# Kernel optimization log

Measured on AMD Instinct MI355X. Metric: run time of the kernel, lower is better.

Reference implementation:

```python
import jax, jax.numpy as jnp
import numpy as np

THETA = 0.7
KS = 3          # deformable-conv kernel size
N = KS * KS     # 9 sampling points


def setup_inputs() -> dict:
    key = jax.random.key(0)
    k = jax.random.split(key, 7)
    B, C, H, W = 2, 256, 64, 64
    x = jax.random.normal(k[0], (B, C, H, W), jnp.float32)
    # offset-predicting conv (3x3, pad 1), 2*N output channels; small init so offsets are sane
    p_w = jax.random.normal(k[1], (2 * N, C, 3, 3), jnp.float32) * 0.01
    p_b = jax.random.normal(k[2], (2 * N,), jnp.float32) * 0.01
    # modulation conv (3x3, pad 1), N output channels
    m_w = jax.random.normal(k[3], (N, C, 3, 3), jnp.float32) * 0.01
    m_b = jnp.zeros((N,), jnp.float32)
    # final deform conv weight (applied as ks x ks, stride ks over the unfolded map), no bias
    dconv_w = jax.random.normal(k[4], (256, C, KS, KS), jnp.float32) * 0.05
    # central-difference conv raw weight, shape (Cout, Cin, 1, 5), no bias
    cdc_w = jax.random.normal(k[5], (256, C, 1, 5), jnp.float32) * 0.05
    return {"x": x, "p_w": p_w, "p_b": p_b, "m_w": m_w, "m_b": m_b,
            "dconv_w": dconv_w, "cdc_w": cdc_w}


def _conv2d(x, w, pad):
    return jax.lax.conv_general_dilated(
        x, w, window_strides=(1, 1), padding=pad,
        dimension_numbers=("NCHW", "OIHW", "NCHW"))


def deform_conv(x, p_w, p_b, m_w, m_b, dconv_w):
    B, C, H, W = x.shape
    same = [(1, 1), (1, 1)]
    offset = _conv2d(x, p_w, same) + p_b[None, :, None, None]          # [B,2N,H,W]
    m = jax.nn.sigmoid(_conv2d(x, m_w, same) + m_b[None, :, None, None])  # [B,N,H,W]

    xp = jnp.pad(x, ((0, 0), (0, 0), (1, 1), (1, 1)))  # zero padding 1
    Hp, Wp = H + 2, W + 2

    # p = p_0 + p_n + offset  (x = row coord, y = col coord; torch meshgrid 'ij')
    p_n_x = jnp.repeat(jnp.arange(-1, 2, dtype=x.dtype), 3)   # [-1,-1,-1,0,0,0,1,1,1]
    p_n_y = jnp.tile(jnp.arange(-1, 2, dtype=x.dtype), 3)     # [-1,0,1,-1,0,1,-1,0,1]
    rows = jnp.arange(1, H + 1, dtype=x.dtype)                # p_0_x
    cols = jnp.arange(1, W + 1, dtype=x.dtype)                # p_0_y
    px = offset[:, :N] + p_n_x[None, :, None, None] + rows[None, None, :, None]
    py = offset[:, N:] + p_n_y[None, :, None, None] + cols[None, None, None, :]
    px = jnp.transpose(px, (0, 2, 3, 1))  # [B,H,W,N]
    py = jnp.transpose(py, (0, 2, 3, 1))

    # integer corners from UNCLAMPED p (detached), as in the original
    fx = jnp.floor(jax.lax.stop_gradient(px))
    fy = jnp.floor(jax.lax.stop_gradient(py))
    qx0 = jnp.clip(fx, 0, Hp - 1)
    qy0 = jnp.clip(fy, 0, Wp - 1)
    qx1 = jnp.clip(fx + 1, 0, Hp - 1)
    qy1 = jnp.clip(fy + 1, 0, Wp - 1)

    # clamp p before computing bilinear weights (original order)
    pxc = jnp.clip(px, 0, Hp - 1)
    pyc = jnp.clip(py, 0, Wp - 1)
    g_lt = (1 + (qx0 - pxc)) * (1 + (qy0 - pyc))
    g_rb = (1 - (qx1 - pxc)) * (1 - (qy1 - pyc))
    g_lb = (1 + (qx0 - pxc)) * (1 - (qy1 - pyc))
    g_rt = (1 - (qx1 - pxc)) * (1 + (qy0 - pyc))

    xf = xp.reshape(B, C, Hp * Wp)

    def gather(qx, qy):
        idx = (qx.astype(jnp.int32) * Wp + qy.astype(jnp.int32)).reshape(B, 1, -1)
        return jnp.take_along_axis(xf, idx, axis=2).reshape(B, C, H, W, N)

    x_off = (g_lt[:, None] * gather(qx0, qy0)
             + g_rb[:, None] * gather(qx1, qy1)
             + g_lb[:, None] * gather(qx0, qy1)
             + g_rt[:, None] * gather(qx1, qy0))          # [B,C,H,W,N]
    x_off = x_off * jnp.transpose(m, (0, 2, 3, 1))[:, None]  # modulation broadcast over C

    # conv(ksxks, stride ks) over the unfolded map == contraction over the N taps;
    # tap n = 3r + c corresponds to kernel position (r, c)
    w = dconv_w.reshape(dconv_w.shape[0], C, N)
    return jnp.einsum("bchwn,ocn->bohw", x_off, w)


def cdc_conv(x, cdc_w):
    Co, Ci = cdc_w.shape[0], cdc_w.shape[1]
    z = jnp.zeros((Co, Ci, 1), cdc_w.dtype)
    wk = jnp.concatenate(
        [z, cdc_w[:, :, :, 0], z, cdc_w[:, :, :, 1], cdc_w[:, :, :, 2],
         cdc_w[:, :, :, 3], z, cdc_w[:, :, :, 4], z], axis=2
    ).reshape(Co, Ci, 3, 3)
    out_normal = _conv2d(x, wk, [(1, 1), (1, 1)])
    kdiff = cdc_w.sum(axis=(2, 3))[:, :, None, None]
    out_diff = _conv2d(x, kdiff, [(0, 0), (0, 0)])
    return out_normal - THETA * out_diff


def reference(x, p_w, p_b, m_w, m_b, dconv_w, cdc_w):
    out_dc = jax.nn.relu(deform_conv(x, p_w, p_b, m_w, m_b, dconv_w))
    out_cdc = jax.nn.relu(cdc_conv(x, cdc_w))
    return jnp.concatenate([out_dc, out_cdc], axis=1)  # [B,512,H,W]
```

## Files before the change

kernel.cpp:

```cpp
#include <hip/hip_runtime.h>
#include <hip/hip_bf16.h>
#include <math.h>

#define XT_BSTRIDE (66*66*256)
#define THETA_ 0.7f

typedef unsigned short u16;
typedef __attribute__((ext_vector_type(8))) short bf16x8;
typedef __attribute__((ext_vector_type(4))) float f32x4;

#define GLOAD16(gp, lp) __builtin_amdgcn_global_load_lds( \
    (const __attribute__((address_space(1))) unsigned int*)(gp), \
    (__attribute__((address_space(3))) unsigned int*)(lp), 16, 0, 0)

__device__ __forceinline__ float bf2f(u16 v) {
  union { unsigned u; float f; } x; x.u = ((unsigned)v) << 16; return x.f;
}
__device__ __forceinline__ u16 f2bf(float f) {
  __hip_bfloat16 h = __float2bfloat16(f);
  return *(u16*)&h;
}

__device__ __forceinline__ size_t swz_idx(int row, int k, int KT) {
  int kt = k >> 6, kc = (k >> 3) & 7, kj = k & 7;
  return (size_t)row * KT + kt * 64 + ((kc ^ (row & 7)) << 3) + kj;
}

__global__ __launch_bounds__(256) void prep(
    const float* __restrict__ x, const float* __restrict__ p_w,
    const float* __restrict__ m_w, const float* __restrict__ dconv_w,
    const float* __restrict__ cdc_w, u16* __restrict__ xTb,
    u16* __restrict__ W1t, u16* __restrict__ Wdt, u16* __restrict__ Wct) {
  int blk = blockIdx.x;
  if (blk < 512) {
    int cg = blk & 3;
    int h  = (blk >> 2) & 63;
    int b  = blk >> 8;
    __shared__ float tile[64][65];
    const float* xp = x + ((size_t)(b * 256 + cg * 64)) * 4096 + h * 64;
#pragma unroll
    for (int j = 0; j < 16; j++) {
      int idx = j * 256 + threadIdx.x;
      int ci = idx >> 6, w = idx & 63;
      tile[ci][w] = xp[(size_t)ci * 4096 + w];
    }
    __syncthreads();
    u16* xo = xTb + (size_t)b * XT_BSTRIDE + ((h + 1) * 66 + 1) * 256 + cg * 64;
#pragma unroll
    for (int j = 0; j < 16; j++) {
      int idx = j * 256 + threadIdx.x;
      int w = idx >> 6, ci = idx & 63;
      xo[(size_t)w * 256 + ci] = f2bf(tile[ci][w]);
    }
    return;
  }
  if (blk < 1032) {
    int i = (blk - 512) * 256 + threadIdx.x;
    if (i >= 133120) return;
    int c = i & 255;
    int j = i >> 8;
    int b = (j >= 260) ? 1 : 0;
    int r = j - b * 260;
    int hp, wp;
    if (r < 66)       { hp = 0;        wp = r; }
    else if (r < 132) { hp = 65;       wp = r - 66; }
    else if (r < 196) { hp = r - 131;  wp = 0; }
    else              { hp = r - 195;  wp = 65; }
    xTb[(size_t)b * XT_BSTRIDE + (hp * 66 + wp) * 256 + c] = 0;
    return;
  }
  int i = (blk - 1032) * 256 + threadIdx.x;
  if (i < 73728) {
    int o = i / 2304, k = i % 2304;
    int kp = k >> 8, c = k & 255;
    float v = 0.f;
    if (o < 18)      v = p_w[((size_t)o * 256 + c) * 9 + kp];
    else if (o < 27) v = m_w[((size_t)(o - 18) * 256 + c) * 9 + kp];
    W1t[swz_idx(o, k, 2304)] = f2bf(v);
    return;
  }
  int j = i - 73728;
  if (j < 589824) {
    int o = j / 2304, k = j % 2304;
    int n = k >> 8, c = k & 255;
    Wdt[swz_idx(o, k, 2304)] = f2bf(dconv_w[((size_t)o * 256 + c) * 9 + n]);
    return;
  }
  int j2 = j - 589824;
  if (j2 < 327680) {
    int o = j2 / 1280, k = j2 % 1280;
    int t = k >> 8, c = k & 255;
    const float* cw = cdc_w + ((size_t)o * 256 + c) * 5;
    float v = cw[t];
    if (t == 2) v -= THETA_ * (cw[0] + cw[1] + cw[2] + cw[3] + cw[4]);
    Wct[swz_idx(o, k, 1280)] = f2bf(v);
  }
}

__global__ __launch_bounds__(256) void sample_params(
    const float* __restrict__ omp, const float* __restrict__ p_b,
    const float* __restrict__ m_b, int4* __restrict__ sidx,
    float4* __restrict__ sg) {
  int i = blockIdx.x * 256 + threadIdx.x;
  if (i >= 73728) return;
  int n = i % 9;
  int p = i / 9;
  int b = p >> 12;
  int hw = p & 4095;
  int h = hw >> 6, w = hw & 63;
  float offx = p_b[n], offy = p_b[9 + n], mraw = m_b[n];
#pragma unroll
  for (int ks = 0; ks < 4; ks++) {
    const float* base = omp + ks * 221184 + b * 110592;
    offx += base[(size_t)n * 4096 + hw];
    offy += base[(size_t)(9 + n) * 4096 + hw];
    mraw += base[(size_t)(18 + n) * 4096 + hw];
  }
  float px = offx + (float)(h + n / 3);
  float py = offy + (float)(w + n % 3);
  float fx = floorf(px), fy = floorf(py);
  float qx0 = fminf(fmaxf(fx, 0.f), 65.f);
  float qy0 = fminf(fmaxf(fy, 0.f), 65.f);
  float qx1 = fminf(fmaxf(fx + 1.f, 0.f), 65.f);
  float qy1 = fminf(fmaxf(fy + 1.f, 0.f), 65.f);
  float pxc = fminf(fmaxf(px, 0.f), 65.f);
  float pyc = fminf(fmaxf(py, 0.f), 65.f);
  float gx0 = 1.f + (qx0 - pxc);
  float gx1 = 1.f - (qx1 - pxc);
  float gy0 = 1.f + (qy0 - pyc);
  float gy1 = 1.f - (qy1 - pyc);
  float m = 1.f / (1.f + expf(-mraw));
  sidx[i] = make_int4((int)qx0 * 66 + (int)qy0, (int)qx1 * 66 + (int)qy1,
                      (int)qx0 * 66 + (int)qy1, (int)qx1 * 66 + (int)qy0);
  sg[i] = make_float4(gx0 * gy0 * m, gx1 * gy1 * m, gx0 * gy1 * m, gx1 * gy0 * m);
}

__global__ __launch_bounds__(256) void gather_Ad(const u16* __restrict__ xTb,
                                                 const int4* __restrict__ sidx,
                                                 const float4* __restrict__ sg,
                                                 u16* __restrict__ Ad) {
  int gid = blockIdx.x * 256 + threadIdx.x;
  int q = gid & 31;
  int s = gid >> 5;
  int p = s / 9, n = s - p * 9;
  int b = p >> 12;
  int4 qi = sidx[s];
  float4 g = sg[s];
  const u16* xb = xTb + (size_t)b * XT_BSTRIDE + q * 8;
  bf16x8 a0 = *(const bf16x8*)(xb + (size_t)qi.x * 256);
  bf16x8 a1 = *(const bf16x8*)(xb + (size_t)qi.y * 256);
  bf16x8 a2 = *(const bf16x8*)(xb + (size_t)qi.z * 256);
  bf16x8 a3 = *(const bf16x8*)(xb + (size_t)qi.w * 256);
  bf16x8 ov;
#pragma unroll
  for (int j = 0; j < 8; j++) {
    float v = g.x * bf2f((u16)a0[j]) + g.y * bf2f((u16)a1[j]) +
              g.z * bf2f((u16)a2[j]) + g.w * bf2f((u16)a3[j]);
    ov[j] = (short)f2bf(v);
  }
  int k = n * 256 + q * 8;
  int kt = k >> 6, kc = (k >> 3) & 7;
  *(bf16x8*)(Ad + (size_t)p * 2304 + kt * 64 + (((kc ^ (p & 7)) << 3))) = ov;
}

template <int KTOT, int MODE>
__device__ __forceinline__ void gemm_body(
    const u16* __restrict__ Asrc, const u16* __restrict__ Bt,
    float* __restrict__ outp, int mt, int nt, int kt0, int nkt,
    u16* As, u16* Bs) {
  const int BN = (MODE == 2) ? 32 : 64;
  const int WM = (MODE == 2) ? 32 : 64;
  const int MF = WM / 16;
  const int OCH0 = (MODE == 1) ? 256 : 0;

  int tid = threadIdx.x;
  int wid = tid >> 6, lane = tid & 63;
  int wr = (MODE == 2) ? wid : (wid >> 1);
  int wc = (MODE == 2) ? 0 : (wid & 1);
  int pbase = mt * 128;
  int obase = nt * BN;
  int l8 = lane >> 3, l7 = lane & 7;
  int lr = lane & 15, lg = lane >> 4;

  f32x4 acc[2][4];
#pragma unroll
  for (int i = 0; i < 2; i++)
#pragma unroll
    for (int j = 0; j < 4; j++) acc[i][j] = {0.f, 0.f, 0.f, 0.f};

  const int dh1[5] = {0, 1, 1, 1, 2}, dw1[5] = {1, 0, 1, 2, 1};

  auto stage = [&](int kt, u16* Ad_, u16* Bd_) {
    if (MODE == 0) {
#pragma unroll
      for (int i = 0; i < 4; i++) {
        int r0 = wid * 32 + i * 8;
        const u16* g = Asrc + (size_t)(pbase + r0 + l8) * KTOT + kt * 64 + (l7 << 3);
        GLOAD16(g, &Ad_[r0 * 64]);
      }
    } else {
      int t = kt >> 2, c0 = (kt & 3) << 6;
      int dh, dw;
      if (MODE == 1) { dh = dh1[t]; dw = dw1[t]; }
      else           { dh = t / 3;  dw = t % 3;  }
#pragma unroll
      for (int i = 0; i < 4; i++) {
        int r0 = wid * 32 + i * 8;
        int r = r0 + l8;
        int p = pbase + r;
        int b = p >> 12, hw = p & 4095, h = hw >> 6, w = hw & 63;
        int chunk = l7 ^ (r & 7);
        const u16* g = Asrc + (size_t)b * XT_BSTRIDE +
                       ((h + dh) * 66 + (w + dw)) * 256 + c0 + (chunk << 3);
        GLOAD16(g, &Ad_[r0 * 64]);
      }
    }
#pragma unroll
    for (int i = 0; i < BN / 32; i++) {
      int o0 = wid * (BN / 4) + i * 8;
      const u16* g = Bt + (size_t)(obase + o0 + l8) * KTOT + kt * 64 + (l7 << 3);
      GLOAD16(g, &Bd_[o0 * 64]);
    }
  };

  stage(kt0, As, Bs);
  __syncthreads();

  for (int it = 0; it < nkt; it++) {
    int cur = it & 1;
    u16* Ac = As + cur * (128 * 64);
    u16* Bc = Bs + cur * (BN * 64);
    if (it + 1 < nkt)
      stage(kt0 + it + 1, As + (cur ^ 1) * (128 * 64), Bs + (cur ^ 1) * (BN * 64));

    bf16x8 av[4][2], bv[2][2];
#pragma unroll
    for (int mf = 0; mf < MF; mf++) {
      int r = wr * WM + mf * 16 + lr;
#pragma unroll
      for (int ks = 0; ks < 2; ks++) {
        int kc = ks * 4 + lg;
        av[mf][ks] = *(const bf16x8*)&Ac[r * 64 + ((kc ^ (r & 7)) << 3)];
      }
    }
#pragma unroll
    for (int nf = 0; nf < 2; nf++) {
      int o = wc * 32 + nf * 16 + lr;
#pragma unroll
      for (int ks = 0; ks < 2; ks++) {
        int kc = ks * 4 + lg;
        bv[nf][ks] = *(const bf16x8*)&Bc[o * 64 + ((kc ^ (o & 7)) << 3)];
      }
    }
#pragma unroll
    for (int nf = 0; nf < 2; nf++)
#pragma unroll
      for (int mf = 0; mf < MF; mf++)
#pragma unroll
        for (int ks = 0; ks < 2; ks++)
          acc[nf][mf] = __builtin_amdgcn_mfma_f32_16x16x32_bf16(
              bv[nf][ks], av[mf][ks], acc[nf][mf], 0, 0, 0);
    __syncthreads();
  }

  if (MODE != 2) {
#pragma unroll
    for (int nf = 0; nf < 2; nf++)
#pragma unroll
      for (int mf = 0; mf < MF; mf++) {
        int p = pbase + wr * WM + mf * 16 + lr;
        int hw = p & 4095, b = p >> 12;
        int og = OCH0 + obase + wc * 32 + nf * 16 + lg * 4;
        f32x4 v = acc[nf][mf];
#pragma unroll
        for (int e = 0; e < 4; e++)
          outp[(size_t)(b * 512 + og + e) * 4096 + hw] = fmaxf(v[e], 0.f);
      }
  } else {
#pragma unroll
    for (int nf = 0; nf < 2; nf++)
#pragma unroll
      for (int mf = 0; mf < 2; mf++) {
        int p = pbase + wr * 32 + mf * 16 + lr;
        int hw = p & 4095, b = p >> 12;
        int o0 = nf * 16 + lg * 4;
        f32x4 v = acc[nf][mf];
#pragma unroll
        for (int e = 0; e < 4; e++) {
          int o = o0 + e;
          if (o < 27)
            outp[(size_t)(b * 27 + o) * 4096 + hw] = v[e];
        }
      }
  }
}

__global__ __launch_bounds__(256) void gemm_offmod(const u16* __restrict__ xTb,
                                                   const u16* __restrict__ W1t,
                                                   float* __restrict__ omp) {
  __shared__ u16 As[2 * 128 * 64];
  __shared__ u16 Bs[2 * 32 * 64];
  int bid = blockIdx.x;
  int xcd = bid & 7;
  int i = bid >> 3;
  int mt = xcd * 8 + (i & 7);
  int ks = i >> 3;
  gemm_body<2304, 2>(xTb, W1t, omp + ks * 221184, mt, 0, ks * 9, 9, As, Bs);
}

__global__ __launch_bounds__(256) void gemm_main(const u16* __restrict__ Ad,
                                                 const u16* __restrict__ xTb,
                                                 const u16* __restrict__ Wdt,
                                                 const u16* __restrict__ Wct,
                                                 float* __restrict__ out) {
  __shared__ u16 As[2 * 128 * 64];
  __shared__ u16 Bs[2 * 64 * 64];
  int bid = blockIdx.x;
  int xcd = bid & 7;
  int i = bid >> 3;
  if (i < 32) {
    int mt = xcd * 8 + (i >> 2);
    int nt = i & 3;
    gemm_body<2304, 0>(Ad, Wdt, out, mt, nt, 0, 36, As, Bs);
  } else {
    i -= 32;
    int mt = xcd * 8 + (i >> 2);
    int nt = i & 3;
    gemm_body<1280, 1>(xTb, Wct, out, mt, nt, 0, 20, As, Bs);
  }
}

extern "C" void kernel_launch(void* const* d_in, const int* in_sizes, int n_in,
                              void* d_out, int out_size, void* d_ws, size_t ws_size,
                              hipStream_t stream) {
  (void)in_sizes; (void)n_in; (void)out_size; (void)ws_size;
  const float* x       = (const float*)d_in[0];
  const float* p_w     = (const float*)d_in[1];
  const float* p_b     = (const float*)d_in[2];
  const float* m_w     = (const float*)d_in[3];
  const float* m_b     = (const float*)d_in[4];
  const float* dconv_w = (const float*)d_in[5];
  const float* cdc_w   = (const float*)d_in[6];
  float* out = (float*)d_out;
  char* ws = (char*)d_ws;

  u16*   xTb  = (u16*)(ws);
  float* omp  = (float*)(ws + 4460544);
  u16*   W1t  = (u16*)(ws + 7999488);
  u16*   Wdt  = (u16*)(ws + 8146944);
  u16*   Wct  = (u16*)(ws + 9326592);
  int4*  sidx = (int4*)(ws + 9981952);
  float4* sg  = (float4*)(ws + 11161600);
  u16*   Ad   = (u16*)(ws + 12341248);

  prep<<<4904, 256, 0, stream>>>(x, p_w, m_w, dconv_w, cdc_w, xTb, W1t, Wdt, Wct);
  gemm_offmod<<<256, 256, 0, stream>>>(xTb, W1t, omp);
  sample_params<<<288, 256, 0, stream>>>(omp, p_b, m_b, sidx, sg);
  gather_Ad<<<9216, 256, 0, stream>>>(xTb, sidx, sg, Ad);
  gemm_main<<<512, 256, 0, stream>>>(Ad, xTb, Wdt, Wct, out);
}
```

Before: 68.82 us.

## Fuse bilinear gather into deform GEMM and retile main GEMMs

Removes the separate gather_Ad kernel and its Ad buffer. Each deform GEMM block now computes the bilinear-sampled, modulated A tile in registers and writes it straight to LDS, overlapping that work with the MFMA loop. The deform path uses 64-row by 256-col tiles, so every gathered A tile feeds all output channels. The CDC path moves to 64x64 tiles, with 640 blocks at two blocks per CU. This avoids writing and re-reading the gathered matrix through global memory and saves a launch, but it puts irregular gather latency inside the GEMM pipeline and raises register pressure.

```diff
diff --git a/kernel.cpp b/kernel.cpp
--- a/kernel.cpp
+++ b/kernel.cpp
@@ -135,91 +135,39 @@
   sg[i] = make_float4(gx0 * gy0 * m, gx1 * gy1 * m, gx0 * gy1 * m, gx1 * gy0 * m);
 }
 
-__global__ __launch_bounds__(256) void gather_Ad(const u16* __restrict__ xTb,
-                                                 const int4* __restrict__ sidx,
-                                                 const float4* __restrict__ sg,
-                                                 u16* __restrict__ Ad) {
-  int gid = blockIdx.x * 256 + threadIdx.x;
-  int q = gid & 31;
-  int s = gid >> 5;
-  int p = s / 9, n = s - p * 9;
-  int b = p >> 12;
-  int4 qi = sidx[s];
-  float4 g = sg[s];
-  const u16* xb = xTb + (size_t)b * XT_BSTRIDE + q * 8;
-  bf16x8 a0 = *(const bf16x8*)(xb + (size_t)qi.x * 256);
-  bf16x8 a1 = *(const bf16x8*)(xb + (size_t)qi.y * 256);
-  bf16x8 a2 = *(const bf16x8*)(xb + (size_t)qi.z * 256);
-  bf16x8 a3 = *(const bf16x8*)(xb + (size_t)qi.w * 256);
-  bf16x8 ov;
-#pragma unroll
-  for (int j = 0; j < 8; j++) {
-    float v = g.x * bf2f((u16)a0[j]) + g.y * bf2f((u16)a1[j]) +
-              g.z * bf2f((u16)a2[j]) + g.w * bf2f((u16)a3[j]);
-    ov[j] = (short)f2bf(v);
-  }
-  int k = n * 256 + q * 8;
-  int kt = k >> 6, kc = (k >> 3) & 7;
-  *(bf16x8*)(Ad + (size_t)p * 2304 + kt * 64 + (((kc ^ (p & 7)) << 3))) = ov;
-}
-
-template <int KTOT, int MODE>
-__device__ __forceinline__ void gemm_body(
-    const u16* __restrict__ Asrc, const u16* __restrict__ Bt,
-    float* __restrict__ outp, int mt, int nt, int kt0, int nkt,
-    u16* As, u16* Bs) {
-  const int BN = (MODE == 2) ? 32 : 64;
-  const int WM = (MODE == 2) ? 32 : 64;
-  const int MF = WM / 16;
-  const int OCH0 = (MODE == 1) ? 256 : 0;
-
+__device__ __forceinline__ void offmod_body(
+    const u16* __restrict__ xTb, const u16* __restrict__ Bt,
+    float* __restrict__ outp, int mt, int kt0, int nkt, u16* As, u16* Bs) {
   int tid = threadIdx.x;
   int wid = tid >> 6, lane = tid & 63;
-  int wr = (MODE == 2) ? wid : (wid >> 1);
-  int wc = (MODE == 2) ? 0 : (wid & 1);
   int pbase = mt * 128;
-  int obase = nt * BN;
   int l8 = lane >> 3, l7 = lane & 7;
   int lr = lane & 15, lg = lane >> 4;
 
-  f32x4 acc[2][4];
+  f32x4 acc[2][2];
 #pragma unroll
   for (int i = 0; i < 2; i++)
 #pragma unroll
-    for (int j = 0; j < 4; j++) acc[i][j] = {0.f, 0.f, 0.f, 0.f};
-
-  const int dh1[5] = {0, 1, 1, 1, 2}, dw1[5] = {1, 0, 1, 2, 1};
-
-  auto stage = [&](int kt, u16* Ad_, u16* Bd_) {
-    if (MODE == 0) {
-#pragma unroll
-      for (int i = 0; i < 4; i++) {
-        int r0 = wid * 32 + i * 8;
-        const u16* g = Asrc + (size_t)(pbase + r0 + l8) * KTOT + kt * 64 + (l7 << 3);
-        GLOAD16(g, &Ad_[r0 * 64]);
-      }
-    } else {
-      int t = kt >> 2, c0 = (kt & 3) << 6;
-      int dh, dw;
-      if (MODE == 1) { dh = dh1[t]; dw = dw1[t]; }
-      else           { dh = t / 3;  dw = t % 3;  }
-#pragma unroll
-      for (int i = 0; i < 4; i++) {
-        int r0 = wid * 32 + i * 8;
-        int r = r0 + l8;
-        int p = pbase + r;
-        int b = p >> 12, hw = p & 4095, h = hw >> 6, w = hw & 63;
-        int chunk = l7 ^ (r & 7);
-        const u16* g = Asrc + (size_t)b * XT_BSTRIDE +
-                       ((h + dh) * 66 + (w + dw)) * 256 + c0 + (chunk << 3);
-        GLOAD16(g, &Ad_[r0 * 64]);
-      }
-    }
-#pragma unroll
-    for (int i = 0; i < BN / 32; i++) {
-      int o0 = wid * (BN / 4) + i * 8;
-      const u16* g = Bt + (size_t)(obase + o0 + l8) * KTOT + kt * 64 + (l7 << 3);
-      GLOAD16(g, &Bd_[o0 * 64]);
+    for (int j = 0; j < 2; j++) acc[i][j] = {0.f, 0.f, 0.f, 0.f};
+
+  auto stage = [&](int kt, u16* Ah, u16* Bh) {
+    int t = kt >> 2, c0 = (kt & 3) << 6;
+    int dh = t / 3, dw = t % 3;
+#pragma unroll
+    for (int i = 0; i < 4; i++) {
+      int r0 = wid * 32 + i * 8;
+      int r = r0 + l8;
+      int p = pbase + r;
+      int b = p >> 12, hw = p & 4095, h = hw >> 6, w = hw & 63;
+      int chunk = l7 ^ (r & 7);
+      const u16* g = xTb + (size_t)b * XT_BSTRIDE +
+                     ((h + dh) * 66 + (w + dw)) * 256 + c0 + (chunk << 3);
+      GLOAD16(g, &Ah[r0 * 64]);
+    }
+    {
+      int o0 = wid * 8;
+      const u16* g = Bt + (size_t)(o0 + l8) * 2304 + kt * 64 + (l7 << 3);
+      GLOAD16(g, &Bh[o0 * 64]);
     }
   };
 
@@ -229,14 +177,14 @@
   for (int it = 0; it < nkt; it++) {
     int cur = it & 1;
     u16* Ac = As + cur * (128 * 64);
-    u16* Bc = Bs + cur * (BN * 64);
+    u16* Bc = Bs + cur * (32 * 64);
     if (it + 1 < nkt)
-      stage(kt0 + it + 1, As + (cur ^ 1) * (128 * 64), Bs + (cur ^ 1) * (BN * 64));
-
-    bf16x8 av[4][2], bv[2][2];
-#pragma unroll
-    for (int mf = 0; mf < MF; mf++) {
-      int r = wr * WM + mf * 16 + lr;
+      stage(kt0 + it + 1, As + (cur ^ 1) * (128 * 64), Bs + (cur ^ 1) * (32 * 64));
+
+    bf16x8 av[2][2], bv[2][2];
+#pragma unroll
+    for (int mf = 0; mf < 2; mf++) {
+      int r = wid * 32 + mf * 16 + lr;
 #pragma unroll
       for (int ks = 0; ks < 2; ks++) {
         int kc = ks * 4 + lg;
@@ -245,7 +193,7 @@
     }
 #pragma unroll
     for (int nf = 0; nf < 2; nf++) {
-      int o = wc * 32 + nf * 16 + lr;
+      int o = nf * 16 + lr;
 #pragma unroll
       for (int ks = 0; ks < 2; ks++) {
         int kc = ks * 4 + lg;
@@ -255,7 +203,7 @@
 #pragma unroll
     for (int nf = 0; nf < 2; nf++)
 #pragma unroll
-      for (int mf = 0; mf < MF; mf++)
+      for (int mf = 0; mf < 2; mf++)
 #pragma unroll
         for (int ks = 0; ks < 2; ks++)
           acc[nf][mf] = __builtin_amdgcn_mfma_f32_16x16x32_bf16(
@@ -263,36 +211,21 @@
     __syncthreads();
   }
 
-  if (MODE != 2) {
-#pragma unroll
-    for (int nf = 0; nf < 2; nf++)
-#pragma unroll
-      for (int mf = 0; mf < MF; mf++) {
-        int p = pbase + wr * WM + mf * 16 + lr;
-        int hw = p & 4095, b = p >> 12;
-        int og = OCH0 + obase + wc * 32 + nf * 16 + lg * 4;
-        f32x4 v = acc[nf][mf];
-#pragma unroll
-        for (int e = 0; e < 4; e++)
-          outp[(size_t)(b * 512 + og + e) * 4096 + hw] = fmaxf(v[e], 0.f);
-      }
-  } else {
-#pragma unroll
-    for (int nf = 0; nf < 2; nf++)
-#pragma unroll
-      for (int mf = 0; mf < 2; mf++) {
-        int p = pbase + wr * 32 + mf * 16 + lr;
-        int hw = p & 4095, b = p >> 12;
-        int o0 = nf * 16 + lg * 4;
-        f32x4 v = acc[nf][mf];
-#pragma unroll
-        for (int e = 0; e < 4; e++) {
-          int o = o0 + e;
-          if (o < 27)
-            outp[(size_t)(b * 27 + o) * 4096 + hw] = v[e];
-        }
-      }
-  }
+#pragma unroll
+  for (int nf = 0; nf < 2; nf++)
+#pragma unroll
+    for (int mf = 0; mf < 2; mf++) {
+      int p = pbase + wid * 32 + mf * 16 + lr;
+      int hw = p & 4095, b = p >> 12;
+      int o0 = nf * 16 + lg * 4;
+      f32x4 v = acc[nf][mf];
+#pragma unroll
+      for (int e = 0; e < 4; e++) {
+        int o = o0 + e;
+        if (o < 27)
+          outp[(size_t)(b * 27 + o) * 4096 + hw] = v[e];
+      }
+    }
 }
 
 __global__ __launch_bounds__(256) void gemm_offmod(const u16* __restrict__ xTb,
@@ -305,28 +238,249 @@
   int i = bid >> 3;
   int mt = xcd * 8 + (i & 7);
   int ks = i >> 3;
-  gemm_body<2304, 2>(xTb, W1t, omp + ks * 221184, mt, 0, ks * 9, 9, As, Bs);
-}
-
-__global__ __launch_bounds__(256) void gemm_main(const u16* __restrict__ Ad,
-                                                 const u16* __restrict__ xTb,
-                                                 const u16* __restrict__ Wdt,
-                                                 const u16* __restrict__ Wct,
-                                                 float* __restrict__ out) {
-  __shared__ u16 As[2 * 128 * 64];
-  __shared__ u16 Bs[2 * 64 * 64];
+  offmod_body(xTb, W1t, omp + ks * 221184, mt, ks * 9, 9, As, Bs);
+}
+
+__device__ void deform_body(const u16* __restrict__ xTb,
+                            const u16* __restrict__ Wdt,
+                            const int4* __restrict__ sidx,
+                            const float4* __restrict__ sg,
+                            float* __restrict__ out, int mt, u16* S) {
+  const int NKT = 36;
+  int tid = threadIdx.x;
+  int wid = tid >> 6, lane = tid & 63;
+  int l8 = lane >> 3, l7 = lane & 7;
+  int lr = lane & 15, lg = lane >> 4;
+  int pbase = mt * 64;
+  int b = pbase >> 12;
+  const u16* xb = xTb + (size_t)b * XT_BSTRIDE;
+
+  int gr = tid >> 2;
+  int gp = pbase + gr;
+  int kc0 = (tid & 3) * 2;
+
+  f32x4 acc[4][4];
+#pragma unroll
+  for (int i = 0; i < 4; i++)
+#pragma unroll
+    for (int j = 0; j < 4; j++) acc[i][j] = {0.f, 0.f, 0.f, 0.f};
+
+  u16* A0 = S;
+  u16* B0 = S + 8192;
+
+  bf16x8 p0, p1;
+  auto gatherA = [&](int kt) {
+    int tap = kt >> 2, c0 = (kt & 3) << 6;
+    int s = gp * 9 + tap;
+    int4 qi = sidx[s];
+    float4 g = sg[s];
+    const u16* xc = xb + c0 + (kc0 << 3);
+    bf16x8 a0 = *(const bf16x8*)(xc + (size_t)qi.x * 256);
+    bf16x8 a1 = *(const bf16x8*)(xc + (size_t)qi.y * 256);
+    bf16x8 a2 = *(const bf16x8*)(xc + (size_t)qi.z * 256);
+    bf16x8 a3 = *(const bf16x8*)(xc + (size_t)qi.w * 256);
+    bf16x8 b0 = *(const bf16x8*)(xc + 8 + (size_t)qi.x * 256);
+    bf16x8 b1 = *(const bf16x8*)(xc + 8 + (size_t)qi.y * 256);
+    bf16x8 b2 = *(const bf16x8*)(xc + 8 + (size_t)qi.z * 256);
+    bf16x8 b3 = *(const bf16x8*)(xc + 8 + (size_t)qi.w * 256);
+#pragma unroll
+    for (int j = 0; j < 8; j++) {
+      float v0 = g.x * bf2f((u16)a0[j]) + g.y * bf2f((u16)a1[j]) +
+                 g.z * bf2f((u16)a2[j]) + g.w * bf2f((u16)a3[j]);
+      float v1 = g.x * bf2f((u16)b0[j]) + g.y * bf2f((u16)b1[j]) +
+                 g.z * bf2f((u16)b2[j]) + g.w * bf2f((u16)b3[j]);
+      p0[j] = (short)f2bf(v0);
+      p1[j] = (short)f2bf(v1);
+    }
+  };
+  auto writeA = [&](u16* Ah) {
+    *(bf16x8*)&Ah[gr * 64 + ((kc0 ^ (gr & 7)) << 3)] = p0;
+    *(bf16x8*)&Ah[gr * 64 + (((kc0 + 1) ^ (gr & 7)) << 3)] = p1;
+  };
+  auto stageB = [&](int kt, u16* Bh) {
+#pragma unroll
+    for (int i = 0; i < 8; i++) {
+      int o0 = wid * 64 + i * 8;
+      const u16* g = Wdt + (size_t)(o0 + l8) * 2304 + kt * 64 + (l7 << 3);
+      GLOAD16(g, &Bh[o0 * 64]);
+    }
+  };
+
+  gatherA(0);
+  writeA(A0);
+  stageB(0, B0);
+  __syncthreads();
+
+  for (int it = 0; it < NKT; it++) {
+    int cur = it & 1;
+    u16* Ac = A0 + cur * 4096;
+    u16* Bc = B0 + cur * 16384;
+    if (it + 1 < NKT) gatherA(it + 1);
+
+    bf16x8 av[4][2], bv[4][2];
+#pragma unroll
+    for (int mf = 0; mf < 4; mf++) {
+      int r = mf * 16 + lr;
+#pragma unroll
+      for (int ks = 0; ks < 2; ks++) {
+        int kc = ks * 4 + lg;
+        av[mf][ks] = *(const bf16x8*)&Ac[r * 64 + ((kc ^ (r & 7)) << 3)];
+      }
+    }
+#pragma unroll
+    for (int nf = 0; nf < 4; nf++) {
+      int o = wid * 64 + nf * 16 + lr;
+#pragma unroll
+      for (int ks = 0; ks < 2; ks++) {
+        int kc = ks * 4 + lg;
+        bv[nf][ks] = *(const bf16x8*)&Bc[o * 64 + ((kc ^ (o & 7)) << 3)];
+      }
+    }
+#pragma unroll
+    for (int nf = 0; nf < 4; nf++)
+#pragma unroll
+      for (int mf = 0; mf < 4; mf++)
+#pragma unroll
+        for (int ks = 0; ks < 2; ks++)
+          acc[nf][mf] = __builtin_amdgcn_mfma_f32_16x16x32_bf16(
+              bv[nf][ks], av[mf][ks], acc[nf][mf], 0, 0, 0);
+
+    if (it + 1 < NKT) {
+      writeA(A0 + (cur ^ 1) * 4096);
+      stageB(it + 1, B0 + (cur ^ 1) * 16384);
+    }
+    __syncthreads();
+  }
+
+#pragma unroll
+  for (int nf = 0; nf < 4; nf++)
+#pragma unroll
+    for (int mf = 0; mf < 4; mf++) {
+      int p = pbase + mf * 16 + lr;
+      int hw = p & 4095;
+      int og = wid * 64 + nf * 16 + lg * 4;
+      f32x4 v = acc[nf][mf];
+#pragma unroll
+      for (int e = 0; e < 4; e++)
+        out[(size_t)(b * 512 + og + e) * 4096 + hw] = fmaxf(v[e], 0.f);
+    }
+}
+
+__device__ void cdc_body(const u16* __restrict__ xTb,
+                         const u16* __restrict__ Wct,
+                         float* __restrict__ out, int mt, int nt, u16* S) {
+  const int NKT = 20;
+  int tid = threadIdx.x;
+  int wid = tid >> 6, lane = tid & 63;
+  int wr = wid >> 1, wc = wid & 1;
+  int l8 = lane >> 3, l7 = lane & 7;
+  int lr = lane & 15, lg = lane >> 4;
+  int pbase = mt * 64;
+  int obase = nt * 64;
+  int b = pbase >> 12;
+
+  f32x4 acc[2][2];
+#pragma unroll
+  for (int i = 0; i < 2; i++)
+#pragma unroll
+    for (int j = 0; j < 2; j++) acc[i][j] = {0.f, 0.f, 0.f, 0.f};
+
+  const int dh1[5] = {0, 1, 1, 1, 2}, dw1[5] = {1, 0, 1, 2, 1};
+  u16* A0 = S;
+  u16* B0 = S + 8192;
+
+  auto stage = [&](int kt, u16* Ah, u16* Bh) {
+    int t = kt >> 2, c0 = (kt & 3) << 6;
+    int dh = dh1[t], dw = dw1[t];
+#pragma unroll
+    for (int i = 0; i < 2; i++) {
+      int r0 = wid * 16 + i * 8;
+      int r = r0 + l8;
+      int p = pbase + r;
+      int hw = p & 4095, h = hw >> 6, w = hw & 63;
+      int chunk = l7 ^ (r & 7);
+      const u16* g = xTb + (size_t)b * XT_BSTRIDE +
+                     ((h + dh) * 66 + (w + dw)) * 256 + c0 + (chunk << 3);
+      GLOAD16(g, &Ah[r0 * 64]);
+    }
+#pragma unroll
+    for (int i = 0; i < 2; i++) {
+      int o0 = wid * 16 + i * 8;
+      const u16* g = Wct + (size_t)(obase + o0 + l8) * 1280 + kt * 64 + (l7 << 3);
+      GLOAD16(g, &Bh[o0 * 64]);
+    }
+  };
+
+  stage(0, A0, B0);
+  __syncthreads();
+
+  for (int it = 0; it < NKT; it++) {
+    int cur = it & 1;
+    u16* Ac = A0 + cur * 4096;
+    u16* Bc = B0 + cur * 4096;
+    if (it + 1 < NKT)
+      stage(it + 1, A0 + (cur ^ 1) * 4096, B0 + (cur ^ 1) * 4096);
+
+    bf16x8 av[2][2], bv[2][2];
+#pragma unroll
+    for (int mf = 0; mf < 2; mf++) {
+      int r = wr * 32 + mf * 16 + lr;
+#pragma unroll
+      for (int ks = 0; ks < 2; ks++) {
+        int kc = ks * 4 + lg;
+        av[mf][ks] = *(const bf16x8*)&Ac[r * 64 + ((kc ^ (r & 7)) << 3)];
+      }
+    }
+#pragma unroll
+    for (int nf = 0; nf < 2; nf++) {
+      int o = wc * 32 + nf * 16 + lr;
+#pragma unroll
+      for (int ks = 0; ks < 2; ks++) {
+        int kc = ks * 4 + lg;
+        bv[nf][ks] = *(const bf16x8*)&Bc[o * 64 + ((kc ^ (o & 7)) << 3)];
+      }
+    }
+#pragma unroll
+    for (int nf = 0; nf < 2; nf++)
+#pragma unroll
+      for (int mf = 0; mf < 2; mf++)
+#pragma unroll
+        for (int ks = 0; ks < 2; ks++)
+          acc[nf][mf] = __builtin_amdgcn_mfma_f32_16x16x32_bf16(
+              bv[nf][ks], av[mf][ks], acc[nf][mf], 0, 0, 0);
+    __syncthreads();
+  }
+
+#pragma unroll
+  for (int nf = 0; nf < 2; nf++)
+#pragma unroll
+    for (int mf = 0; mf < 2; mf++) {
+      int p = pbase + wr * 32 + mf * 16 + lr;
+      int hw = p & 4095;
+      int og = 256 + obase + wc * 32 + nf * 16 + lg * 4;
+      f32x4 v = acc[nf][mf];
+#pragma unroll
+      for (int e = 0; e < 4; e++)
+        out[(size_t)(b * 512 + og + e) * 4096 + hw] = fmaxf(v[e], 0.f);
+    }
+}
+
+__global__ __launch_bounds__(256, 2) void gemm_main(
+    const u16* __restrict__ xTb, const u16* __restrict__ Wdt,
+    const u16* __restrict__ Wct, const int4* __restrict__ sidx,
+    const float4* __restrict__ sg, float* __restrict__ out) {
+  __shared__ u16 S[40960];
   int bid = blockIdx.x;
-  int xcd = bid & 7;
-  int i = bid >> 3;
-  if (i < 32) {
-    int mt = xcd * 8 + (i >> 2);
-    int nt = i & 3;
-    gemm_body<2304, 0>(Ad, Wdt, out, mt, nt, 0, 36, As, Bs);
+  if (bid < 128) {
+    int mt = (bid & 7) * 16 + (bid >> 3);
+    deform_body(xTb, Wdt, sidx, sg, out, mt, S);
   } else {
-    i -= 32;
-    int mt = xcd * 8 + (i >> 2);
-    int nt = i & 3;
-    gemm_body<1280, 1>(xTb, Wct, out, mt, nt, 0, 20, As, Bs);
+    int i = bid - 128;
+    int xcd = i & 7;
+    int j = i >> 3;
+    int mt = xcd * 16 + (j & 15);
+    int nt = j >> 4;
+    cdc_body(xTb, Wct, out, mt, nt, S);
   }
 }
 
@@ -351,11 +505,9 @@
   u16*   Wct  = (u16*)(ws + 9326592);
   int4*  sidx = (int4*)(ws + 9981952);
   float4* sg  = (float4*)(ws + 11161600);
-  u16*   Ad   = (u16*)(ws + 12341248);
 
   prep<<<4904, 256, 0, stream>>>(x, p_w, m_w, dconv_w, cdc_w, xTb, W1t, Wdt, Wct);
   gemm_offmod<<<256, 256, 0, stream>>>(xTb, W1t, omp);
   sample_params<<<288, 256, 0, stream>>>(omp, p_b, m_b, sidx, sg);
-  gather_Ad<<<9216, 256, 0, stream>>>(xTb, sidx, sg, Ad);
-  gemm_main<<<512, 256, 0, stream>>>(Ad, xTb, Wdt, Wct, out);
-}
+  gemm_main<<<640, 256, 0, stream>>>(xTb, Wdt, Wct, sidx, sg, out);
+}
```

Result: slower. 80.35 us (+16.8%).
